# Kernel tuning notes

Hardware: AMD Instinct MI355X
Metric: run time of the kernel (lower is better)

## Reference

```python
import jax, jax.numpy as jnp
import numpy as np

ALPHA = 0.01
TOP_K = 2
N_EXPERTS = 8

def setup_inputs() -> dict:
    key = jax.random.key(0)
    k1, k2 = jax.random.split(key)
    hidden_states = jax.random.normal(k1, (4, 4096, 2048), dtype=jnp.float32)
    # kaiming_uniform_(a=sqrt(5)) on [E, H] -> bound = sqrt(6/((1+5)*H)) = 1/sqrt(H)
    bound = 1.0 / np.sqrt(2048.0)
    weight = jax.random.uniform(k2, (N_EXPERTS, 2048), dtype=jnp.float32,
                                minval=-bound, maxval=bound)
    return {"hidden_states": hidden_states, "weight": weight}

def reference(hidden_states, weight):
    bsz, seq_len, h = hidden_states.shape
    x = hidden_states.reshape(-1, h)                      # [T, H], T = bsz*seq_len
    logits = jnp.einsum('th,eh->te', x, weight)           # [T, E]
    scores = jax.nn.softmax(logits, axis=-1)              # [T, E]
    topk_weight, topk_idx = jax.lax.top_k(scores, TOP_K)  # [T, K], [T, K]
    # aux load-balancing loss (training, seq_aux=False)
    flat_idx = topk_idx.reshape(-1)                       # [T*K]
    counts = jnp.zeros((N_EXPERTS,), dtype=jnp.float32).at[flat_idx].add(1.0)
    ce = counts / flat_idx.shape[0]                       # mean of one-hots
    Pi = scores.mean(axis=0)                              # [E]
    fi = ce * N_EXPERTS
    aux_loss = jnp.sum(Pi * fi) * ALPHA
    return topk_idx, topk_weight, aux_loss
```

## Files before the change

kernel.cpp:

```cpp
#include <hip/hip_runtime.h>

#define T_TOK 16384
#define H 2048
#define HV (H / 4)
#define NE 8
#define TPG 4
#define WPB 8
#define ALPHA 0.01f
#define TOPK 2
#define NBLK 512


__global__ __launch_bounds__(512, 4) void gate_main(
    const float* __restrict__ x, const float* __restrict__ w,
    float* __restrict__ out, float* __restrict__ ws)
{
    __shared__ float wl[NE * H];
    __shared__ float s_pi[NE];
    __shared__ float s_cnt[NE];

    const int tid  = threadIdx.x;
    const int lane = tid & 63;
    const int wave = tid >> 6;
    const int t0   = (blockIdx.x * WPB + wave) * TPG;

    const float4* __restrict__ xv = (const float4*)x;
    const float4* __restrict__ wv = (const float4*)w;

    const float4* xp = xv + (size_t)t0 * HV + lane;
    float4 xa[TPG], xb[TPG];
#pragma unroll
    for (int t = 0; t < TPG; t++) xa[t] = xp[t * HV];

    float4* wl4 = (float4*)wl;
#pragma unroll
    for (int k = 0; k < 8; k++) wl4[tid + k * 512] = wv[tid + k * 512];
    if (tid < NE) { s_pi[tid] = 0.f; s_cnt[tid] = 0.f; }
    __syncthreads();

    float acc[NE][TPG];
#pragma unroll
    for (int e = 0; e < NE; e++)
#pragma unroll
        for (int t = 0; t < TPG; t++) acc[e][t] = 0.f;

    const float4* wlv = (const float4*)wl;

#pragma unroll
    for (int j = 0; j < 8; j += 2) {
#pragma unroll
        for (int t = 0; t < TPG; t++) xb[t] = xp[t * HV + (j + 1) * 64];
#pragma unroll
        for (int e = 0; e < NE; e++) {
            const float4 wr = wlv[e * HV + j * 64 + lane];
#pragma unroll
            for (int t = 0; t < TPG; t++) {
                acc[e][t] = fmaf(xa[t].x, wr.x, acc[e][t]);
                acc[e][t] = fmaf(xa[t].y, wr.y, acc[e][t]);
                acc[e][t] = fmaf(xa[t].z, wr.z, acc[e][t]);
                acc[e][t] = fmaf(xa[t].w, wr.w, acc[e][t]);
            }
        }
        if (j + 2 < 8) {
#pragma unroll
            for (int t = 0; t < TPG; t++) xa[t] = xp[t * HV + (j + 2) * 64];
        }
#pragma unroll
        for (int e = 0; e < NE; e++) {
            const float4 wr = wlv[e * HV + (j + 1) * 64 + lane];
#pragma unroll
            for (int t = 0; t < TPG; t++) {
                acc[e][t] = fmaf(xb[t].x, wr.x, acc[e][t]);
                acc[e][t] = fmaf(xb[t].y, wr.y, acc[e][t]);
                acc[e][t] = fmaf(xb[t].z, wr.z, acc[e][t]);
                acc[e][t] = fmaf(xb[t].w, wr.w, acc[e][t]);
            }
        }
    }

#pragma unroll
    for (int e = 0; e < NE; e++)
#pragma unroll
        for (int t = 0; t < TPG; t++) {
            float v = acc[e][t];
#pragma unroll
            for (int off = 32; off >= 1; off >>= 1)
                v += __shfl_xor(v, off, 64);
            acc[e][t] = v;
        }

    float pi_loc[NE], cnt_loc[NE];
#pragma unroll
    for (int e = 0; e < NE; e++) { pi_loc[e] = 0.f; cnt_loc[e] = 0.f; }

#pragma unroll
    for (int t = 0; t < TPG; t++) {
        float l[NE];
#pragma unroll
        for (int e = 0; e < NE; e++) l[e] = acc[e][t];
        float m = l[0];
#pragma unroll
        for (int e = 1; e < NE; e++) m = fmaxf(m, l[e]);
        float s[NE];
        float sum = 0.f;
#pragma unroll
        for (int e = 0; e < NE; e++) { s[e] = __expf(l[e] - m); sum += s[e]; }
#pragma unroll
        for (int e = 0; e < NE; e++) s[e] = s[e] / sum;

        float b1 = -1.f, b2 = -1.f;
        int   i1 = 0,    i2 = 0;
#pragma unroll
        for (int e = 0; e < NE; e++) {
            if (s[e] > b1) { b2 = b1; i2 = i1; b1 = s[e]; i1 = e; }
            else if (s[e] > b2) { b2 = s[e]; i2 = e; }
        }

        if (lane == t) {
            const int tok = t0 + t;
            out[tok * 2 + 0]             = (float)i1;
            out[tok * 2 + 1]             = (float)i2;
            out[2 * T_TOK + tok * 2 + 0] = b1;
            out[2 * T_TOK + tok * 2 + 1] = b2;
        }
        const float sel = (lane == t) ? 1.f : 0.f;
#pragma unroll
        for (int e = 0; e < NE; e++) {
            pi_loc[e]  += sel * s[e];
            cnt_loc[e] += sel * (((i1 == e) ? 1.f : 0.f) + ((i2 == e) ? 1.f : 0.f));
        }
    }

    if (lane < TPG) {
#pragma unroll
        for (int e = 0; e < NE; e++) {
            atomicAdd(&s_pi[e],  pi_loc[e]);
            atomicAdd(&s_cnt[e], cnt_loc[e]);
        }
    }
    __syncthreads();
    if (tid < NE) {
        ws[blockIdx.x * 16 + tid]     = s_pi[tid];
        ws[blockIdx.x * 16 + 8 + tid] = s_cnt[tid];
    }
}

__global__ __launch_bounds__(256) void gate_aux(
    const float* __restrict__ ws, float* __restrict__ out)
{
    __shared__ float s_pi[NE];
    __shared__ float s_cnt[NE];
    const int tid = threadIdx.x;
    if (tid < NE) { s_pi[tid] = 0.f; s_cnt[tid] = 0.f; }
    __syncthreads();

    float pi[NE], cnt[NE];
#pragma unroll
    for (int e = 0; e < NE; e++) { pi[e] = 0.f; cnt[e] = 0.f; }

    for (int b = tid; b < NBLK; b += 256) {
        const float4* p = (const float4*)(ws + b * 16);
        float4 a0 = p[0], a1 = p[1], a2 = p[2], a3 = p[3];
        pi[0] += a0.x; pi[1] += a0.y; pi[2] += a0.z; pi[3] += a0.w;
        pi[4] += a1.x; pi[5] += a1.y; pi[6] += a1.z; pi[7] += a1.w;
        cnt[0] += a2.x; cnt[1] += a2.y; cnt[2] += a2.z; cnt[3] += a2.w;
        cnt[4] += a3.x; cnt[5] += a3.y; cnt[6] += a3.z; cnt[7] += a3.w;
    }

#pragma unroll
    for (int e = 0; e < NE; e++) {
#pragma unroll
        for (int off = 32; off >= 1; off >>= 1) {
            pi[e]  += __shfl_xor(pi[e],  off, 64);
            cnt[e] += __shfl_xor(cnt[e], off, 64);
        }
    }
    if ((tid & 63) == 0) {
#pragma unroll
        for (int e = 0; e < NE; e++) {
            atomicAdd(&s_pi[e],  pi[e]);
            atomicAdd(&s_cnt[e], cnt[e]);
        }
    }
    __syncthreads();

    if (tid == 0) {
        float aux = 0.f;
#pragma unroll
        for (int e = 0; e < NE; e++) {
            const float Pi = s_pi[e] / (float)T_TOK;
            const float ce = s_cnt[e] / (float)(T_TOK * TOPK);
            aux += Pi * ce * (float)NE;
        }
        out[4 * T_TOK] = aux * ALPHA;
    }
}

extern "C" void kernel_launch(void* const* d_in, const int* in_sizes, int n_in,
                              void* d_out, int out_size, void* d_ws, size_t ws_size,
                              hipStream_t stream) {
    const float* x = (const float*)d_in[0];
    const float* w = (const float*)d_in[1];
    float* out = (float*)d_out;
    float* ws  = (float*)d_ws;

    gate_main<<<NBLK, 512, 0, stream>>>(x, w, out, ws);
    gate_aux<<<1, 256, 0, stream>>>(ws, out);
}
```

Measured before the change: 204.4 us.

## Load gate weights straight into LDS and deepen x prefetch pipeline

Weight staging now uses global_load_lds to copy from global memory into LDS directly, so the data no longer passes through registers. The x loop is restructured to prefetch two chunks ahead into separate register buffers, which keeps more loads in flight. Per-block aux statistics are reduced with per-wave shared slots instead of LDS atomics, and top-k outputs are written as float2 stores. The deeper prefetch raises register pressure under the existing launch bounds, which may lower occupancy or cause spills.

```diff
diff --git a/kernel.cpp b/kernel.cpp
--- a/kernel.cpp
+++ b/kernel.cpp
@@ -10,14 +10,31 @@
 #define TOPK 2
 #define NBLK 512
 
+#define GAS __attribute__((address_space(1)))
+#define LAS __attribute__((address_space(3)))
+
+
+#define COMPUTE_J(xr, jj)                                               \
+    {                                                                   \
+        _Pragma("unroll")                                               \
+        for (int e = 0; e < NE; e++) {                                  \
+            const float4 wr = wlv[e * HV + (jj) * 64 + lane];           \
+            _Pragma("unroll")                                           \
+            for (int t = 0; t < TPG; t++) {                             \
+                acc[e][t] = fmaf(xr[t].x, wr.x, acc[e][t]);             \
+                acc[e][t] = fmaf(xr[t].y, wr.y, acc[e][t]);             \
+                acc[e][t] = fmaf(xr[t].z, wr.z, acc[e][t]);             \
+                acc[e][t] = fmaf(xr[t].w, wr.w, acc[e][t]);             \
+            }                                                           \
+        }                                                               \
+    }
 
 __global__ __launch_bounds__(512, 4) void gate_main(
     const float* __restrict__ x, const float* __restrict__ w,
     float* __restrict__ out, float* __restrict__ ws)
 {
     __shared__ float wl[NE * H];
-    __shared__ float s_pi[NE];
-    __shared__ float s_cnt[NE];
+    __shared__ float s_part[WPB * 16];
 
     const int tid  = threadIdx.x;
     const int lane = tid & 63;
@@ -26,16 +43,21 @@
 
     const float4* __restrict__ xv = (const float4*)x;
     const float4* __restrict__ wv = (const float4*)w;
-
     const float4* xp = xv + (size_t)t0 * HV + lane;
+
     float4 xa[TPG], xb[TPG];
 #pragma unroll
     for (int t = 0; t < TPG; t++) xa[t] = xp[t * HV];
+#pragma unroll
+    for (int t = 0; t < TPG; t++) xb[t] = xp[t * HV + 64];
 
     float4* wl4 = (float4*)wl;
 #pragma unroll
-    for (int k = 0; k < 8; k++) wl4[tid + k * 512] = wv[tid + k * 512];
-    if (tid < NE) { s_pi[tid] = 0.f; s_cnt[tid] = 0.f; }
+    for (int k = 0; k < 8; k++) {
+        __builtin_amdgcn_global_load_lds(
+            (const GAS void*)(wv + tid + k * 512),
+            (LAS void*)(wl4 + tid + k * 512), 16, 0, 0);
+    }
     __syncthreads();
 
     float acc[NE][TPG];
@@ -48,33 +70,24 @@
 
 #pragma unroll
     for (int j = 0; j < 8; j += 2) {
-#pragma unroll
-        for (int t = 0; t < TPG; t++) xb[t] = xp[t * HV + (j + 1) * 64];
-#pragma unroll
-        for (int e = 0; e < NE; e++) {
-            const float4 wr = wlv[e * HV + j * 64 + lane];
-#pragma unroll
-            for (int t = 0; t < TPG; t++) {
-                acc[e][t] = fmaf(xa[t].x, wr.x, acc[e][t]);
-                acc[e][t] = fmaf(xa[t].y, wr.y, acc[e][t]);
-                acc[e][t] = fmaf(xa[t].z, wr.z, acc[e][t]);
-                acc[e][t] = fmaf(xa[t].w, wr.w, acc[e][t]);
-            }
-        }
+        float4 xn[TPG], xm[TPG];
         if (j + 2 < 8) {
 #pragma unroll
-            for (int t = 0; t < TPG; t++) xa[t] = xp[t * HV + (j + 2) * 64];
-        }
-#pragma unroll
-        for (int e = 0; e < NE; e++) {
-            const float4 wr = wlv[e * HV + (j + 1) * 64 + lane];
-#pragma unroll
-            for (int t = 0; t < TPG; t++) {
-                acc[e][t] = fmaf(xb[t].x, wr.x, acc[e][t]);
-                acc[e][t] = fmaf(xb[t].y, wr.y, acc[e][t]);
-                acc[e][t] = fmaf(xb[t].z, wr.z, acc[e][t]);
-                acc[e][t] = fmaf(xb[t].w, wr.w, acc[e][t]);
-            }
+            for (int t = 0; t < TPG; t++) xn[t] = xp[t * HV + (j + 2) * 64];
+        }
+        COMPUTE_J(xa, j);
+        if (j + 3 < 8) {
+#pragma unroll
+            for (int t = 0; t < TPG; t++) xm[t] = xp[t * HV + (j + 3) * 64];
+        }
+        COMPUTE_J(xb, j + 1);
+        if (j + 2 < 8) {
+#pragma unroll
+            for (int t = 0; t < TPG; t++) xa[t] = xn[t];
+        }
+        if (j + 3 < 8) {
+#pragma unroll
+            for (int t = 0; t < TPG; t++) xb[t] = xm[t];
         }
     }
 
@@ -118,30 +131,29 @@
 
         if (lane == t) {
             const int tok = t0 + t;
-            out[tok * 2 + 0]             = (float)i1;
-            out[tok * 2 + 1]             = (float)i2;
-            out[2 * T_TOK + tok * 2 + 0] = b1;
-            out[2 * T_TOK + tok * 2 + 1] = b2;
-        }
-        const float sel = (lane == t) ? 1.f : 0.f;
-#pragma unroll
-        for (int e = 0; e < NE; e++) {
-            pi_loc[e]  += sel * s[e];
-            cnt_loc[e] += sel * (((i1 == e) ? 1.f : 0.f) + ((i2 == e) ? 1.f : 0.f));
-        }
-    }
-
-    if (lane < TPG) {
-#pragma unroll
-        for (int e = 0; e < NE; e++) {
-            atomicAdd(&s_pi[e],  pi_loc[e]);
-            atomicAdd(&s_cnt[e], cnt_loc[e]);
-        }
-    }
-    __syncthreads();
-    if (tid < NE) {
-        ws[blockIdx.x * 16 + tid]     = s_pi[tid];
-        ws[blockIdx.x * 16 + 8 + tid] = s_cnt[tid];
+            ((float2*)out)[tok]               = make_float2((float)i1, (float)i2);
+            ((float2*)(out + 2 * T_TOK))[tok] = make_float2(b1, b2);
+        }
+#pragma unroll
+        for (int e = 0; e < NE; e++) {
+            pi_loc[e]  += s[e];
+            cnt_loc[e] += ((i1 == e) ? 1.f : 0.f) + ((i2 == e) ? 1.f : 0.f);
+        }
+    }
+
+    if (lane == 0) {
+#pragma unroll
+        for (int e = 0; e < NE; e++) {
+            s_part[wave * 16 + e]     = pi_loc[e];
+            s_part[wave * 16 + 8 + e] = cnt_loc[e];
+        }
+    }
+    __syncthreads();
+    if (tid < 16) {
+        float v = 0.f;
+#pragma unroll
+        for (int wv8 = 0; wv8 < WPB; wv8++) v += s_part[wv8 * 16 + tid];
+        ws[blockIdx.x * 16 + tid] = v;
     }
 }
 
```

After: 201.0 us (median of 2 runs). Within noise of the previous version (-1.7%).
